# Kernel optimization log

Hardware: AMD Instinct MI355X
Metric: run time of the kernel (lower is better)

The kernel has to match this reference:

```python
import jax, jax.numpy as jnp
import numpy as np

D_MODEL = 1024
D_HEAD = 64
N_HEADS = D_MODEL // D_HEAD
MAX_SEQ = 2048
BATCH = 2
SEQ = 2048


def setup_inputs() -> dict:
    key = jax.random.key(0)
    ks = jax.random.split(key, 10)
    s = 1.0 / np.sqrt(D_MODEL)
    return {
        "x": jax.random.normal(ks[0], (BATCH, SEQ, D_MODEL), dtype=jnp.float32),
        "Wq": jax.random.normal(ks[1], (D_MODEL, D_MODEL), dtype=jnp.float32) * s,
        "bq": jax.random.normal(ks[2], (D_MODEL,), dtype=jnp.float32) * 0.01,
        "Wk": jax.random.normal(ks[3], (D_MODEL, D_MODEL), dtype=jnp.float32) * s,
        "bk": jax.random.normal(ks[4], (D_MODEL,), dtype=jnp.float32) * 0.01,
        "Wv": jax.random.normal(ks[5], (D_MODEL, D_MODEL), dtype=jnp.float32) * s,
        "bv": jax.random.normal(ks[6], (D_MODEL,), dtype=jnp.float32) * 0.01,
        "Er": jax.random.normal(ks[7], (MAX_SEQ, D_HEAD), dtype=jnp.float32),
        "Wo": jax.random.normal(ks[8], (D_MODEL, D_MODEL), dtype=jnp.float32) * s,
        "bo": jax.random.normal(ks[9], (D_MODEL,), dtype=jnp.float32) * 0.01,
    }


def _s_rel(q, Er):
    # q: [B,H,S,Dh]; use last S rows of Er (start = max_seq - seq)
    S = q.shape[2]
    Er_slice = Er[Er.shape[0] - S:, :]                  # [S, Dh]
    qE = jnp.einsum("bhsd,ld->bhsl", q, Er_slice)       # [B,H,S,S]
    padded = jnp.pad(qE, ((0, 0), (0, 0), (0, 0), (1, 0)))  # [B,H,S,S+1]
    B, H, S1, S2 = padded.shape
    padded = padded.reshape(B, H, S2, S1)               # skew trick
    return padded[:, :, 1:, :]                          # [B,H,S,S]


def reference(x, Wq, bq, Wk, bk, Wv, bv, Er, Wo, bo):
    B, S, _ = x.shape
    scale = 1.0 / np.sqrt(D_HEAD)
    # projections (torch Linear: x @ W.T + b)
    def proj(W, b):
        return (x @ W.T + b).reshape(B, S, N_HEADS, D_HEAD).transpose(0, 2, 1, 3)
    q = proj(Wq, bq)   # [B,H,S,Dh]
    k = proj(Wk, bk)
    v = proj(Wv, bv)
    qk = jnp.einsum("bhsd,bhtd->bhst", q, k)            # [B,H,S,S]
    logits = (qk + _s_rel(q, Er)) * scale
    causal = jnp.tril(jnp.ones((S, S), dtype=bool))
    masked = jnp.where(causal[None, None], logits, -1e9)
    attn = jax.nn.softmax(masked, axis=-1)
    out = jnp.einsum("bhst,bhtd->bhsd", attn, v)        # [B,H,S,Dh]
    out = out.transpose(0, 2, 1, 3).reshape(B, S, D_MODEL)
    return out @ Wo.T + bo
```

## Files before the change

### kernel.cpp

```cpp
#include <hip/hip_runtime.h>
#include <hip/hip_bf16.h>

typedef short v8s __attribute__((ext_vector_type(8)));
typedef float v4f __attribute__((ext_vector_type(4)));
typedef __hip_bfloat16 bf16;
typedef unsigned int u32;

#define MFMA(a, b, c) __builtin_amdgcn_mfma_f32_16x16x32_bf16(a, b, c, 0, 0, 0)

__device__ __forceinline__ void gload16(const bf16* g, bf16* l) {
    __builtin_amdgcn_global_load_lds(
        (const __attribute__((address_space(1))) u32*)(g),
        (__attribute__((address_space(3))) u32*)(l), 16, 0, 0);
}

__global__ __launch_bounds__(256) void cast_all(
    const float* __restrict__ x,  const float* __restrict__ wq,
    const float* __restrict__ wk, const float* __restrict__ wv,
    const float* __restrict__ wo, const float* __restrict__ er,
    bf16* __restrict__ xb,  bf16* __restrict__ wqb, bf16* __restrict__ wkb,
    bf16* __restrict__ wvb, bf16* __restrict__ wob, bf16* __restrict__ erb)
{
    const int r = blockIdx.y;
    const float* s; bf16* d; int n4;
    if      (r == 0) { s = x;  d = xb;  n4 = 1048576; }
    else if (r == 1) { s = wq; d = wqb; n4 = 262144;  }
    else if (r == 2) { s = wk; d = wkb; n4 = 262144;  }
    else if (r == 3) { s = wv; d = wvb; n4 = 262144;  }
    else if (r == 4) { s = wo; d = wob; n4 = 262144;  }
    else             { s = er; d = erb; n4 = 32768;   }
    const int i = blockIdx.x * 256 + threadIdx.x;
    if (i < n4) {
        const float4 v = ((const float4*)s)[i];
        bf16 t[4];
        t[0] = __float2bfloat16(v.x);
        t[1] = __float2bfloat16(v.y);
        t[2] = __float2bfloat16(v.z);
        t[3] = __float2bfloat16(v.w);
        ((uint2*)d)[i] = *(const uint2*)t;
    }
}

__global__ __launch_bounds__(256) void gemm_nt(
    const bf16* __restrict__ A, const bf16* __restrict__ W,
    const float* __restrict__ b0, const float* __restrict__ b1,
    const float* __restrict__ b2,
    bf16* __restrict__ oHM, bf16* __restrict__ Vt, float* __restrict__ outf)
{
    __shared__ bf16 As[2][128 * 64];
    __shared__ bf16 Bs[2][128 * 64];

    const int tid = threadIdx.x;
    const int w  = tid >> 6, l = tid & 63;
    const int lm = l & 15,  lq = l >> 4;
    const int wm = (w >> 1) * 64, wn = (w & 1) * 64;
    const int m0 = blockIdx.y * 128, n0 = blockIdx.x * 128;

    const int grow = l >> 3;
    const int gcol = ((l & 7) ^ grow) * 8;

    v4f acc[4][4];
#pragma unroll
    for (int i = 0; i < 4; ++i)
#pragma unroll
        for (int j = 0; j < 4; ++j) acc[i][j] = (v4f){0.f, 0.f, 0.f, 0.f};

    const int sw = (lm & 7) << 4;

    auto STAGE = [&](int p, int k0) {
#pragma unroll
        for (int q = 0; q < 4; ++q) {
            const int rr = w * 32 + q * 8;
            gload16(&A[(size_t)(m0 + rr + grow) * 1024 + k0 + gcol], &As[p][rr * 64]);
            gload16(&W[(size_t)(n0 + rr + grow) * 1024 + k0 + gcol], &Bs[p][rr * 64]);
        }
    };
    auto COMPUTE = [&](int p) {
#pragma unroll
        for (int kk = 0; kk < 2; ++kk) {
            v8s a[4], b[4];
            const int cb = (lq * 16 + kk * 64);
#pragma unroll
            for (int i = 0; i < 4; ++i) {
                const int row = wm + i * 16 + lm;
                a[i] = *(const v8s*)((const char*)As[p] + row * 128 + (cb ^ sw));
            }
#pragma unroll
            for (int j = 0; j < 4; ++j) {
                const int row = wn + j * 16 + lm;
                b[j] = *(const v8s*)((const char*)Bs[p] + row * 128 + (cb ^ sw));
            }
#pragma unroll
            for (int i = 0; i < 4; ++i)
#pragma unroll
                for (int j = 0; j < 4; ++j)
                    acc[i][j] = MFMA(b[j], a[i], acc[i][j]);
        }
    };

    STAGE(0, 0);
    __syncthreads();
    for (int t = 0; t < 15; ++t) {
        STAGE((t + 1) & 1, (t + 1) * 64);
        COMPUTE(t & 1);
        __syncthreads();
    }
    COMPUTE(1);

    const int z = blockIdx.x >> 3;
    const float* bias = (z == 0) ? b0 : (z == 1) ? b1 : b2;

    float4 bj[4];
#pragma unroll
    for (int j = 0; j < 4; ++j)
        bj[j] = *(const float4*)&bias[(n0 & 1023) + wn + j * 16 + lq * 4];

#pragma unroll
    for (int i = 0; i < 4; ++i) {
        const int row = m0 + wm + i * 16 + lm;
        const int bb = row >> 11, ss = row & 2047;
#pragma unroll
        for (int j = 0; j < 4; ++j) {
            const int cc = (n0 & 1023) + wn + j * 16 + lq * 4;
            const float v0 = acc[i][j][0] + bj[j].x;
            const float v1 = acc[i][j][1] + bj[j].y;
            const float v2 = acc[i][j][2] + bj[j].z;
            const float v3 = acc[i][j][3] + bj[j].w;
            if (outf) {
                const float4 fv = {v0, v1, v2, v3};
                *(float4*)&outf[(size_t)row * 1024 + cc] = fv;
            } else {
                bf16 t[4];
                t[0] = __float2bfloat16(v0);
                t[1] = __float2bfloat16(v1);
                t[2] = __float2bfloat16(v2);
                t[3] = __float2bfloat16(v3);
                const int hh = cc >> 6, dd = cc & 63;
                if (z < 2) {
                    *(uint2*)&oHM[(size_t)z * 4194304 +
                        ((size_t)(bb * 16 + hh) * 2048 + ss) * 64 + dd] = *(uint2*)t;
                } else {
#pragma unroll
                    for (int r = 0; r < 4; ++r)
                        Vt[((size_t)(bb * 16 + hh) * 64 + dd + r) * 2048 + ss] = t[r];
                }
            }
        }
    }
}

__device__ const unsigned char QBt[48] = {
    31,31,30,15, 30,29,29,28,14, 28,27,27,26,13, 26,25,25,24,12,
    24,23,23,22,11, 22,21,21,20,10, 20,19,19,18,9, 18,17,17,16,8,
    16,7, 6,5,4,3,2,1,0};
__device__ const unsigned char TTt[48] = {
     0, 1, 0, 2,  1, 0, 1, 0, 2,  1, 0, 1, 0, 2,  1, 0, 1, 0, 2,
     1, 0, 1, 0, 2,  1, 0, 1, 0, 2,  1, 0, 1, 0, 2,  1, 0, 1, 0, 2,
     1, 2, 2,2,2,2,2,2,2};

__global__ __launch_bounds__(256, 4) void attn(
    const bf16* __restrict__ Q, const bf16* __restrict__ K,
    const bf16* __restrict__ Vt, const bf16* __restrict__ Er,
    bf16* __restrict__ AO, float* __restrict__ Opart, float* __restrict__ dpart)
{
    __shared__ bf16 Ks[64 * 72];
    __shared__ bf16 Vs[64 * 72];
    __shared__ bf16 Gs2[64 * 104];

    const int ord = blockIdx.x;
    const int bh = ord & 31;
    const int s  = ord >> 5;
    const int qb = QBt[s];
    const int tt = TTt[s];
    const int t0   = (tt == 2) ? 0 : tt;
    const int step = (tt == 2) ? 1 : 2;
    const int slot = (tt == 2) ? -1 : (((qb - 16) * 32 + bh) * 2 + tt);

    const int i0 = qb * 64;
    const int b  = bh >> 4, h = bh & 15;
    const int tid = threadIdx.x;
    const int w  = tid >> 6, l = tid & 63;
    const int lm = l & 15,  lq = l >> 4;

    const bf16* qp = Q + ((size_t)bh * 2048 + i0 + w * 16 + lm) * 64 + lq * 8;
    const v8s q0 = *(const v8s*)qp;
    const v8s q1f = *(const v8s*)(qp + 32);

    v4f accO[4];
#pragma unroll
    for (int dt = 0; dt < 4; ++dt) accO[dt] = (v4f){0.f, 0.f, 0.f, 0.f};
    float rsc = 0.f;

    const int sr0 = tid >> 3;
    const int sc8 = (tid & 7) * 8;
    const size_t kbase = (size_t)bh * 2048 * 64;
    const size_t vbase = (size_t)bh * 64 * 2048;

    const int grow_g = (w * 16 + lm) * 104;
    const int ig     = i0 + w * 16 + lm;

    const int jt0 = t0 * 64;
    uint4 kp0 = *(const uint4*)&K[kbase + (size_t)(jt0 + sr0) * 64 + sc8];
    uint4 kp1 = *(const uint4*)&K[kbase + (size_t)(jt0 + sr0 + 32) * 64 + sc8];
    uint4 vp0 = *(const uint4*)&Vt[vbase + (size_t)sr0 * 2048 + jt0 + sc8];
    uint4 vp1 = *(const uint4*)&Vt[vbase + (size_t)(sr0 + 32) * 2048 + jt0 + sc8];

    for (int it = t0; it <= qb; it += step) {
        const int j0 = it * 64;
        __syncthreads();
        *(uint4*)&Ks[sr0 * 72 + sc8]        = kp0;
        *(uint4*)&Ks[(sr0 + 32) * 72 + sc8] = kp1;
        *(uint4*)&Vs[sr0 * 72 + sc8]        = vp0;
        *(uint4*)&Vs[(sr0 + 32) * 72 + sc8] = vp1;
        if (it + step <= qb) {
            const int jn = j0 + step * 64;
            kp0 = *(const uint4*)&K[kbase + (size_t)(jn + sr0) * 64 + sc8];
            kp1 = *(const uint4*)&K[kbase + (size_t)(jn + sr0 + 32) * 64 + sc8];
            vp0 = *(const uint4*)&Vt[vbase + (size_t)sr0 * 2048 + jn + sc8];
            vp1 = *(const uint4*)&Vt[vbase + (size_t)(sr0 + 32) * 2048 + jn + sc8];
        }
        const int basew = 2048 - 16 - i0 + j0 - 16 * w;
#pragma unroll
        for (int ct2 = 0; ct2 < 5; ++ct2) {
            int mr = basew + ct2 * 16 + lm;
            mr = (mr > 2047) ? 2047 : mr;
            const bf16* ep = Er + (size_t)mr * 64 + lq * 8;
            const v8s e0 = *(const v8s*)ep;
            const v8s e1 = *(const v8s*)(ep + 32);
            v4f g = (v4f){0.f, 0.f, 0.f, 0.f};
            g = MFMA(e0, q0, g);
            g = MFMA(e1, q1f, g);
            const int cb = ct2 * 16 + lq * 4 + lm + 1;
#pragma unroll
            for (int r = 0; r < 4; ++r)
                Gs2[grow_g + cb + r] = __float2bfloat16(g[r] * 0.125f);
        }
        __syncthreads();
        v4f sv[4];
#pragma unroll
        for (int ct = 0; ct < 4; ++ct) {
            const v8s k0f = *(const v8s*)&Ks[(ct * 16 + lm) * 72 + lq * 8];
            const v8s k1f = *(const v8s*)&Ks[(ct * 16 + lm) * 72 + 32 + lq * 8];
            v4f s2 = (v4f){0.f, 0.f, 0.f, 0.f};
            s2 = MFMA(k0f, q0, s2);
            s2 = MFMA(k1f, q1f, s2);
            sv[ct] = s2;
        }
#pragma unroll
        for (int ct = 0; ct < 4; ++ct) {
            const uint2 graw = *(const uint2*)&Gs2[grow_g + 16 + ct * 16 + lq * 4];
            const bf16* gb4 = (const bf16*)&graw;
            bf16 pt[4];
#pragma unroll
            for (int r = 0; r < 4; ++r) {
                const int jj = ct * 16 + lq * 4 + r;
                float sc = fmaf(sv[ct][r], 0.125f, (float)gb4[r]);
                if (j0 + jj > ig) sc = -1e9f;
                const float pe = __expf(sc - 4.0f);
                rsc += pe;
                pt[r] = __float2bfloat16(pe);
            }
            *(uint2*)&Gs2[grow_g + ct * 16 + lq * 4] = *(const uint2*)pt;
        }
        const v8s pa0 = *(const v8s*)&Gs2[grow_g + lq * 8];
        const v8s pa1 = *(const v8s*)&Gs2[grow_g + 32 + lq * 8];
#pragma unroll
        for (int dt = 0; dt < 4; ++dt) {
            const v8s vb0 = *(const v8s*)&Vs[(dt * 16 + lm) * 72 + lq * 8];
            const v8s vb1 = *(const v8s*)&Vs[(dt * 16 + lm) * 72 + 32 + lq * 8];
            accO[dt] = MFMA(pa0, vb0, accO[dt]);
            accO[dt] = MFMA(pa1, vb1, accO[dt]);
        }
    }
    rsc += __shfl_xor(rsc, 16, 64);
    rsc += __shfl_xor(rsc, 32, 64);
    float den[4];
#pragma unroll
    for (int r = 0; r < 4; ++r) den[r] = __shfl(rsc, lq * 4 + r, 64);

    if (slot < 0) {
#pragma unroll
        for (int dt = 0; dt < 4; ++dt) {
#pragma unroll
            for (int r = 0; r < 4; ++r) {
                const int row = i0 + w * 16 + lq * 4 + r;
                const int d   = dt * 16 + lm;
                AO[((size_t)b * 2048 + row) * 1024 + h * 64 + d] =
                    __float2bfloat16(accO[dt][r] / den[r]);
            }
        }
    } else {
        float* op = Opart + (size_t)slot * 4096;
#pragma unroll
        for (int dt = 0; dt < 4; ++dt) {
#pragma unroll
            for (int r = 0; r < 4; ++r) {
                const int row = w * 16 + lq * 4 + r;
                op[row * 64 + dt * 16 + lm] = accO[dt][r];
            }
        }
        if (lm == 0) {
#pragma unroll
            for (int r = 0; r < 4; ++r)
                dpart[slot * 64 + w * 16 + lq * 4 + r] = den[r];
        }
    }
}

__global__ __launch_bounds__(256) void fixup(
    const float* __restrict__ Opart, const float* __restrict__ dpart,
    bf16* __restrict__ AO)
{
    const int pi = blockIdx.x;
    const int qb = 16 + (pi >> 5);
    const int bh = pi & 31;
    const int b = bh >> 4, h = bh & 15;
    const int t = threadIdx.x;
    const int row = t >> 2;
    const int c0 = (t & 3) * 16;
    const float dA = dpart[(pi * 2) * 64 + row];
    const float dB = dpart[(pi * 2 + 1) * 64 + row];
    const float inv = 1.0f / (dA + dB);
    const float* A = Opart + (size_t)(pi * 2) * 4096 + row * 64 + c0;
    const float* B = Opart + (size_t)(pi * 2 + 1) * 4096 + row * 64 + c0;
    bf16* dst = AO + ((size_t)b * 2048 + qb * 64 + row) * 1024 + h * 64 + c0;
#pragma unroll
    for (int c = 0; c < 16; c += 4) {
        bf16 tt[4];
#pragma unroll
        for (int r = 0; r < 4; ++r)
            tt[r] = __float2bfloat16((A[c + r] + B[c + r]) * inv);
        *(uint2*)&dst[c] = *(uint2*)tt;
    }
}

extern "C" void kernel_launch(void* const* d_in, const int* in_sizes, int n_in,
                              void* d_out, int out_size, void* d_ws, size_t ws_size,
                              hipStream_t stream)
{
    const float* x  = (const float*)d_in[0];
    const float* Wq = (const float*)d_in[1];
    const float* bq = (const float*)d_in[2];
    const float* Wk = (const float*)d_in[3];
    const float* bk = (const float*)d_in[4];
    const float* Wv = (const float*)d_in[5];
    const float* bv = (const float*)d_in[6];
    const float* Er = (const float*)d_in[7];
    const float* Wo = (const float*)d_in[8];
    const float* bo = (const float*)d_in[9];
    float* out = (float*)d_out;

    bf16* ws = (bf16*)d_ws;
    const size_t NEl = (size_t)4096 * 1024;
    bf16* Qw  = ws;
    bf16* Kw  = ws + NEl;
    bf16* Vtw = ws + 3 * NEl;
    bf16* xb  = ws + 4 * NEl;
    bf16* AOw = xb;
    bf16* Wqb = ws + 5 * NEl;
    bf16* Wkb = Wqb + 1024 * 1024;
    bf16* Wvb = Wkb + 1024 * 1024;
    bf16* Wob = Wvb + 1024 * 1024;
    bf16* Erb = Wob + 1024 * 1024;
    float* dpart = (float*)(Erb + (size_t)2048 * 64);
    float* Opart = out;
    (void)Kw;

    cast_all<<<dim3(4096, 6), 256, 0, stream>>>(x, Wq, Wk, Wv, Wo, Er,
                                                xb, Wqb, Wkb, Wvb, Wob, Erb);
    gemm_nt<<<dim3(24, 32), 256, 0, stream>>>(xb, Wqb, bq, bk, bv, Qw, Vtw, nullptr);
    attn<<<dim3(1536), 256, 0, stream>>>(Qw, Kw, Vtw, Erb, AOw, Opart, dpart);
    fixup<<<dim3(512), 256, 0, stream>>>(Opart, dpart, AOw);
    gemm_nt<<<dim3(8, 32), 256, 0, stream>>>(AOw, Wob, bo, bo, bo, nullptr, nullptr, out);
}
```

Before: 275.3 us.

## Double-buffer K/V tiles in LDS and drop mid-iteration barrier in attention

The attention kernel now keeps two LDS buffers for the K and V tiles. While the current tile is being consumed, the register-prefetched next tile is written into the other buffer. This removes the second __syncthreads per iteration and leaves only a compiler memory fence, relying on the G scratch rows being private to each wave. The cost is roughly 18 KB more LDS per block, and launch bounds drop from 4 to 3 blocks per CU, which lowers occupancy.

```diff
diff --git a/kernel.cpp b/kernel.cpp
--- a/kernel.cpp
+++ b/kernel.cpp
@@ -158,13 +158,13 @@
      1, 0, 1, 0, 2,  1, 0, 1, 0, 2,  1, 0, 1, 0, 2,  1, 0, 1, 0, 2,
      1, 2, 2,2,2,2,2,2,2};
 
-__global__ __launch_bounds__(256, 4) void attn(
+__global__ __launch_bounds__(256, 3) void attn(
     const bf16* __restrict__ Q, const bf16* __restrict__ K,
     const bf16* __restrict__ Vt, const bf16* __restrict__ Er,
     bf16* __restrict__ AO, float* __restrict__ Opart, float* __restrict__ dpart)
 {
-    __shared__ bf16 Ks[64 * 72];
-    __shared__ bf16 Vs[64 * 72];
+    __shared__ bf16 Ks[2][64 * 72];
+    __shared__ bf16 Vs[2][64 * 72];
     __shared__ bf16 Gs2[64 * 104];
 
     const int ord = blockIdx.x;
@@ -175,6 +175,7 @@
     const int t0   = (tt == 2) ? 0 : tt;
     const int step = (tt == 2) ? 1 : 2;
     const int slot = (tt == 2) ? -1 : (((qb - 16) * 32 + bh) * 2 + tt);
+    const int N    = (qb - t0) / step + 1;
 
     const int i0 = qb * 64;
     const int b  = bh >> 4, h = bh & 15;
@@ -199,25 +200,45 @@
     const int grow_g = (w * 16 + lm) * 104;
     const int ig     = i0 + w * 16 + lm;
 
-    const int jt0 = t0 * 64;
-    uint4 kp0 = *(const uint4*)&K[kbase + (size_t)(jt0 + sr0) * 64 + sc8];
-    uint4 kp1 = *(const uint4*)&K[kbase + (size_t)(jt0 + sr0 + 32) * 64 + sc8];
-    uint4 vp0 = *(const uint4*)&Vt[vbase + (size_t)sr0 * 2048 + jt0 + sc8];
-    uint4 vp1 = *(const uint4*)&Vt[vbase + (size_t)(sr0 + 32) * 2048 + jt0 + sc8];
-
-    for (int it = t0; it <= qb; it += step) {
+    {
+        const int jt0 = t0 * 64;
+        const uint4 a0 = *(const uint4*)&K[kbase + (size_t)(jt0 + sr0) * 64 + sc8];
+        const uint4 a1 = *(const uint4*)&K[kbase + (size_t)(jt0 + sr0 + 32) * 64 + sc8];
+        const uint4 c0 = *(const uint4*)&Vt[vbase + (size_t)sr0 * 2048 + jt0 + sc8];
+        const uint4 c1 = *(const uint4*)&Vt[vbase + (size_t)(sr0 + 32) * 2048 + jt0 + sc8];
+        *(uint4*)&Ks[0][sr0 * 72 + sc8]        = a0;
+        *(uint4*)&Ks[0][(sr0 + 32) * 72 + sc8] = a1;
+        *(uint4*)&Vs[0][sr0 * 72 + sc8]        = c0;
+        *(uint4*)&Vs[0][(sr0 + 32) * 72 + sc8] = c1;
+    }
+    uint4 kp0, kp1, vp0, vp1;
+    if (N > 1) {
+        const int jn = (t0 + step) * 64;
+        kp0 = *(const uint4*)&K[kbase + (size_t)(jn + sr0) * 64 + sc8];
+        kp1 = *(const uint4*)&K[kbase + (size_t)(jn + sr0 + 32) * 64 + sc8];
+        vp0 = *(const uint4*)&Vt[vbase + (size_t)sr0 * 2048 + jn + sc8];
+        vp1 = *(const uint4*)&Vt[vbase + (size_t)(sr0 + 32) * 2048 + jn + sc8];
+    }
+
+    for (int n = 0; n < N; ++n) {
+        const int it = t0 + n * step;
         const int j0 = it * 64;
+        const int p  = n & 1;
         __syncthreads();
-        *(uint4*)&Ks[sr0 * 72 + sc8]        = kp0;
-        *(uint4*)&Ks[(sr0 + 32) * 72 + sc8] = kp1;
-        *(uint4*)&Vs[sr0 * 72 + sc8]        = vp0;
-        *(uint4*)&Vs[(sr0 + 32) * 72 + sc8] = vp1;
-        if (it + step <= qb) {
-            const int jn = j0 + step * 64;
-            kp0 = *(const uint4*)&K[kbase + (size_t)(jn + sr0) * 64 + sc8];
-            kp1 = *(const uint4*)&K[kbase + (size_t)(jn + sr0 + 32) * 64 + sc8];
-            vp0 = *(const uint4*)&Vt[vbase + (size_t)sr0 * 2048 + jn + sc8];
-            vp1 = *(const uint4*)&Vt[vbase + (size_t)(sr0 + 32) * 2048 + jn + sc8];
+        if (n + 1 < N) {
+            bf16* kd = Ks[p ^ 1];
+            bf16* vd = Vs[p ^ 1];
+            *(uint4*)&kd[sr0 * 72 + sc8]        = kp0;
+            *(uint4*)&kd[(sr0 + 32) * 72 + sc8] = kp1;
+            *(uint4*)&vd[sr0 * 72 + sc8]        = vp0;
+            *(uint4*)&vd[(sr0 + 32) * 72 + sc8] = vp1;
+            if (n + 2 < N) {
+                const int jn = (it + 2 * step) * 64;
+                kp0 = *(const uint4*)&K[kbase + (size_t)(jn + sr0) * 64 + sc8];
+                kp1 = *(const uint4*)&K[kbase + (size_t)(jn + sr0 + 32) * 64 + sc8];
+                vp0 = *(const uint4*)&Vt[vbase + (size_t)sr0 * 2048 + jn + sc8];
+                vp1 = *(const uint4*)&Vt[vbase + (size_t)(sr0 + 32) * 2048 + jn + sc8];
+            }
         }
         const int basew = 2048 - 16 - i0 + j0 - 16 * w;
 #pragma unroll
@@ -235,12 +256,12 @@
             for (int r = 0; r < 4; ++r)
                 Gs2[grow_g + cb + r] = __float2bfloat16(g[r] * 0.125f);
         }
-        __syncthreads();
+        asm volatile("" ::: "memory");
         v4f sv[4];
 #pragma unroll
         for (int ct = 0; ct < 4; ++ct) {
-            const v8s k0f = *(const v8s*)&Ks[(ct * 16 + lm) * 72 + lq * 8];
-            const v8s k1f = *(const v8s*)&Ks[(ct * 16 + lm) * 72 + 32 + lq * 8];
+            const v8s k0f = *(const v8s*)&Ks[p][(ct * 16 + lm) * 72 + lq * 8];
+            const v8s k1f = *(const v8s*)&Ks[p][(ct * 16 + lm) * 72 + 32 + lq * 8];
             v4f s2 = (v4f){0.f, 0.f, 0.f, 0.f};
             s2 = MFMA(k0f, q0, s2);
             s2 = MFMA(k1f, q1f, s2);
@@ -266,8 +287,8 @@
         const v8s pa1 = *(const v8s*)&Gs2[grow_g + 32 + lq * 8];
 #pragma unroll
         for (int dt = 0; dt < 4; ++dt) {
-            const v8s vb0 = *(const v8s*)&Vs[(dt * 16 + lm) * 72 + lq * 8];
-            const v8s vb1 = *(const v8s*)&Vs[(dt * 16 + lm) * 72 + 32 + lq * 8];
+            const v8s vb0 = *(const v8s*)&Vs[p][(dt * 16 + lm) * 72 + lq * 8];
+            const v8s vb1 = *(const v8s*)&Vs[p][(dt * 16 + lm) * 72 + 32 + lq * 8];
             accO[dt] = MFMA(pa0, vb0, accO[dt]);
             accO[dt] = MFMA(pa1, vb1, accO[dt]);
         }
```

Measured after the change: 270.4 us (median of 2 runs). About the same (-1.8%).
